# Kernel tuning notes

Hardware: AMD Instinct MI355X
Metric: run time of the kernel (lower is better)

## Reference

```python
import jax, jax.numpy as jnp
import numpy as np

B, L, D_IN = 4, 2048, 80
D, H, DFF, WIN = 128, 16, 128, 64
DH = D // H
BN_EPS = 1e-5


def sinusoidal_positional_encoding(l, d, dtype):
    # Faithful to source: pos_j = 10000 ** (j / d) (exponent j/d, not 2j/d)
    n = d // 2 + (d % 2 == 1)
    pos_i = jnp.arange(l, dtype=dtype)[:, None]                  # [L,1]
    pos_j = jnp.power(jnp.asarray(10000.0, dtype), jnp.arange(n, dtype=dtype) / d)  # [n]
    ang = pos_i / pos_j                                          # [L,n]
    pos = jnp.stack([jnp.sin(ang), jnp.cos(ang)], axis=-1).reshape(l, -1)
    return pos[:, :d]                                            # [L,D]


def local_window_disallowed_mask(l, win):
    # Source: mask starts as ones (True = disallowed), zeros only strictly
    i = jnp.arange(l)
    diff = jnp.abs(i[:, None] - i[None, :])
    allowed = (diff >= 1) & (diff <= win)
    return ~allowed                                              # [L,L] bool, True = masked


def setup_inputs() -> dict:
    key = jax.random.key(0)
    ks = jax.random.split(key, 17)
    s = 0.05  # weight scale for numerical stability
    return {
        "x": jax.random.normal(ks[0], (B, L, D_IN), jnp.float32),
        "conv_w": jax.random.normal(ks[1], (D, D_IN), jnp.float32) * s,
        "conv_b": jax.random.normal(ks[2], (D,), jnp.float32) * s,
        "bn_g": jax.random.uniform(ks[3], (D,), jnp.float32, 0.5, 1.5),
        "bn_b": jax.random.normal(ks[4], (D,), jnp.float32) * s,
        "bn_rm": jax.random.normal(ks[5], (D,), jnp.float32) * s,
        "bn_rv": jax.random.uniform(ks[6], (D,), jnp.float32, 0.5, 1.5),
        "in_proj_w": jax.random.normal(ks[7], (3 * D, D), jnp.float32) * s,
        "in_proj_b": jax.random.normal(ks[8], (3 * D,), jnp.float32) * s,
        "out_w": jax.random.normal(ks[9], (D, D), jnp.float32) * s,
        "out_b": jax.random.normal(ks[10], (D,), jnp.float32) * s,
        "ff_w1": jax.random.normal(ks[11], (DFF, D), jnp.float32) * s,
        "ff_b1": jax.random.normal(ks[12], (DFF,), jnp.float32) * s,
        "ff_w2": jax.random.normal(ks[13], (D, DFF), jnp.float32) * s,
        "ff_b2": jax.random.normal(ks[14], (D,), jnp.float32) * s,
        "fc_w": jax.random.normal(ks[15], (D_IN, D), jnp.float32) * s,
        "fc_b": jax.random.normal(ks[16], (D_IN,), jnp.float32) * s,
    }


def _forward(x, conv_w, conv_b, bn_g, bn_b, bn_rm, bn_rv,
             in_proj_w, in_proj_b, out_w, out_b,
             ff_w1, ff_b1, ff_w2, ff_b2, fc_w, fc_b):
    b, l, _ = x.shape
    dt = x.dtype
    # Conv1d(kernel=1) + ReLU + BatchNorm1d (eval mode, running stats)
    h = jax.nn.relu(jnp.einsum('bli,oi->blo', x, conv_w) + conv_b)     # [B,L,D]
    h = (h - bn_rm) * (bn_g * jax.lax.rsqrt(bn_rv + BN_EPS)) + bn_b
    # positional encoding
    h = h + sinusoidal_positional_encoding(l, D, dt)
    # MultiheadAttention (torch semantics: joint in_proj, scaled dot, out_proj)
    qkv = jnp.einsum('bld,ed->ble', h, in_proj_w) + in_proj_b          # [B,L,3D]
    q, k, v = jnp.split(qkv, 3, axis=-1)
    q = q.reshape(b, l, H, DH).transpose(0, 2, 1, 3)                   # [B,H,L,dh]
    k = k.reshape(b, l, H, DH).transpose(0, 2, 1, 3)
    v = v.reshape(b, l, H, DH).transpose(0, 2, 1, 3)
    scores = jnp.einsum('bhqd,bhkd->bhqk', q, k) / jnp.sqrt(jnp.asarray(DH, dt))
    mask = local_window_disallowed_mask(l, WIN)                        # True = masked
    scores = jnp.where(mask, jnp.finfo(dt).min, scores)
    attn = jax.nn.softmax(scores, axis=-1)                             # [B,H,L,L]
    ctx = jnp.einsum('bhqk,bhkd->bhqd', attn, v)
    ctx = ctx.transpose(0, 2, 1, 3).reshape(b, l, D)
    attn_out = jnp.einsum('bld,od->blo', ctx, out_w) + out_b           # [B,L,D]
    # FFN (no residual in source)
    f = jax.nn.relu(jnp.einsum('bld,fd->blf', attn_out, ff_w1) + ff_b1)
    f = jnp.einsum('blf,df->bld', f, ff_w2) + ff_b2                    # [B,L,D]
    # final head
    return jnp.einsum('bld,od->blo', f, fc_w) + fc_b                   # [B,L,80]


def reference(x, conv_w, conv_b, bn_g, bn_b, bn_rm, bn_rv,
              in_proj_w, in_proj_b, out_w, out_b,
              ff_w1, ff_b1, ff_w2, ff_b2, fc_w, fc_b):
    return _forward(x, conv_w, conv_b, bn_g, bn_b, bn_rm, bn_rv,
                    in_proj_w, in_proj_b, out_w, out_b,
                    ff_w1, ff_b1, ff_w2, ff_b2, fc_w, fc_b)
```

## Files before the change

### kernel.cpp

```cpp
#include <hip/hip_runtime.h>
#include <hip/hip_bf16.h>
#include <math.h>

constexpr int B_ = 4, L_ = 2048, DIN = 80, D_ = 128, H_ = 16, DH = 8;
constexpr int T_ = B_ * L_;
constexpr int LDX = T_;

__device__ float g_xT  [DIN * T_];
__device__ float g_posT[D_ * L_];
__device__ float g_h   [D_ * T_];
__device__ float g_ctx [D_ * T_];
__device__ float g_f1  [D_ * T_];
__device__ float g_q3  [B_ * H_ * L_ * DH];
__device__ float g_k3  [B_ * H_ * L_ * DH];
__device__ float g_v3  [B_ * H_ * L_ * DH];
__device__ float g_WconvT[DIN * D_];
__device__ float g_WqkvT [D_ * 3 * D_];
__device__ float g_Wf1T  [D_ * D_];
__device__ float g_WfcT  [D_ * D_];
__device__ float g_bf1   [D_];
__device__ float g_bfc   [D_];

__global__ void prep_fold(const float* __restrict__ x,
                          const float* __restrict__ conv_w,
                          const float* __restrict__ in_proj_w,
                          const float* __restrict__ out_w,
                          const float* __restrict__ out_b,
                          const float* __restrict__ ff_w1,
                          const float* __restrict__ ff_b1,
                          const float* __restrict__ ff_w2,
                          const float* __restrict__ ff_b2,
                          const float* __restrict__ fc_w,
                          const float* __restrict__ fc_b) {
    __shared__ float rowbuf[2][128];
    __shared__ float red[256];
    int bid = blockIdx.x, tid = threadIdx.x;

    if (bid < 512) {
        int idx = bid * 256 + tid;
        int l = idx >> 6, j = idx & 63;
        double ang = (double)l * exp((double)j * (-9.210340371976184 / 128.0));
        g_posT[(2 * j) * L_ + l]     = (float)sin(ang);
        g_posT[(2 * j + 1) * L_ + l] = (float)cos(ang);
        return;
    }
    if (bid < 3072) {
        int e = (bid - 512) * 256 + tid;
        int t = e / 80, k = e - t * 80;
        g_xT[k * T_ + t] = x[e];
        return;
    }
    if (bid < 3112) {
        int e = (bid - 3072) * 256 + tid;
        int o = e / 80, k = e - o * 80;
        g_WconvT[k * D_ + o] = conv_w[e];
        return;
    }
    if (bid < 3304) {
        int e = (bid - 3112) * 256 + tid;
        int o = e >> 7, k = e & 127;
        g_WqkvT[k * (3 * D_) + o] = in_proj_w[e];
        return;
    }
    if (bid < 3368) {
        int sub = tid >> 7, k = tid & 127;
        int f = (bid - 3304) * 2 + sub;
        rowbuf[sub][k] = ff_w1[f * 128 + k];
        __syncthreads();
        float acc = 0.f;
#pragma unroll 8
        for (int o = 0; o < 128; o++)
            acc = fmaf(rowbuf[sub][o], out_w[o * 128 + k], acc);
        g_Wf1T[k * 128 + f] = acc;
        red[tid] = rowbuf[sub][k] * out_b[k];
        __syncthreads();
        for (int s = 64; s > 0; s >>= 1) {
            if (k < s) red[tid] += red[tid + s];
            __syncthreads();
        }
        if (k == 0) g_bf1[f] = red[sub * 128] + ff_b1[f];
        return;
    }
    {
        int sub = tid >> 7, k = tid & 127;
        int o = (bid - 3368) * 2 + sub;
        rowbuf[sub][k] = (o < 80) ? fc_w[o * 128 + k] : 0.f;
        __syncthreads();
        float acc = 0.f;
#pragma unroll 8
        for (int d = 0; d < 128; d++)
            acc = fmaf(rowbuf[sub][d], ff_w2[d * 128 + k], acc);
        g_WfcT[k * 128 + o] = acc;
        red[tid] = rowbuf[sub][k] * ff_b2[k];
        __syncthreads();
        for (int s = 64; s > 0; s >>= 1) {
            if (k < s) red[tid] += red[tid + s];
            __syncthreads();
        }
        if (k == 0) g_bfc[o] = (o < 80) ? (red[sub * 128] + fc_b[o]) : 0.f;
        return;
    }
}

template <int K, int LDW, int EPI>
__global__ __launch_bounds__(256) void gemm_kernel(
        const float* __restrict__ X, const float* __restrict__ Wt,
        const float* __restrict__ bias,
        const float* __restrict__ bg, const float* __restrict__ bb,
        const float* __restrict__ brm, const float* __restrict__ brv,
        float* __restrict__ Y) {
    __shared__ float Xs[K][64];
    __shared__ float Ws[K][64];
    int tid = threadIdx.x;
    int t0 = blockIdx.x * 64;
    int cb = blockIdx.y * 64;
    int tc = tid & 15, tr = tid >> 4;

    for (int i = tid; i < K * 16; i += 256) {
        int k = i >> 4, f = i & 15;
        *(float4*)&Xs[k][f * 4] = *(const float4*)&X[(size_t)k * LDX + t0 + f * 4];
    }
    for (int i = tid; i < K * 16; i += 256) {
        int k = i >> 4, f = i & 15;
        *(float4*)&Ws[k][f * 4] = *(const float4*)&Wt[(size_t)k * LDW + cb + f * 4];
    }
    __syncthreads();

    float acc[4][4] = {};
#pragma unroll 4
    for (int k = 0; k < K; ++k) {
        float4 a = *(float4*)&Xs[k][tr * 4];
        float4 w = *(float4*)&Ws[k][tc * 4];
        float av[4] = {a.x, a.y, a.z, a.w};
        float wv[4] = {w.x, w.y, w.z, w.w};
#pragma unroll
        for (int i = 0; i < 4; i++)
#pragma unroll
            for (int jj = 0; jj < 4; jj++)
                acc[i][jj] = fmaf(av[i], wv[jj], acc[i][jj]);
    }

    if (EPI == 3) {
#pragma unroll
        for (int i = 0; i < 4; i++) {
            int t = t0 + tr * 4 + i;
            int b = t >> 11, l = t & 2047;
#pragma unroll
            for (int jj = 0; jj < 4; jj++) {
                int C = cb + tc * 4 + jj;
                float v = acc[i][jj] + bias[C];
                int slab = C >> 7, cs = C & 127;
                float* dst = (slab == 0) ? g_q3 : (slab == 1 ? g_k3 : g_v3);
                dst[(((size_t)(b * H_ + (cs >> 3))) * L_ + l) * DH + (cs & 7)] = v;
            }
        }
        return;
    }
    if (EPI == 4) {
#pragma unroll
        for (int i = 0; i < 4; i++) {
            int t = t0 + tr * 4 + i;
            int c0 = cb + tc * 4;
            if (c0 < 80) {
                float vs[4];
#pragma unroll
                for (int jj = 0; jj < 4; jj++) vs[jj] = acc[i][jj] + bias[c0 + jj];
                *(float4*)&Y[(size_t)t * 80 + c0] = *(float4*)vs;
            }
        }
        return;
    }
#pragma unroll
    for (int jj = 0; jj < 4; jj++) {
        int c = cb + tc * 4 + jj;
        float bv = bias[c];
        float vs[4];
#pragma unroll
        for (int i = 0; i < 4; i++) {
            float v = acc[i][jj] + bv;
            if (EPI == 1) v = fmaxf(v, 0.0f);
            if (EPI == 2) {
                v = fmaxf(v, 0.0f);
                v = (v - brm[c]) * (bg[c] * rsqrtf(brv[c] + 1e-5f)) + bb[c];
                v += g_posT[c * L_ + ((t0 + tr * 4) & 2047) + i];
            }
            vs[i] = v;
        }
        *(float4*)&Y[(size_t)c * LDX + t0 + tr * 4] = *(float4*)vs;
    }
}

__global__ __launch_bounds__(128) void attn_kernel() {
    __shared__ float Ks[385 * 8];
    __shared__ float Vs[385 * 8];
    int bh = blockIdx.x;
    int qb = blockIdx.y * 256;
    int tid = threadIdx.x;
    int kbase = qb - 64;

    const float* kgl = g_k3 + (size_t)bh * L_ * DH;
    const float* vgl = g_v3 + (size_t)bh * L_ * DH;
    const float* qgl = g_q3 + (size_t)bh * L_ * DH;

    for (int i = tid; i < 385 * 2; i += 128) {
        int li = i >> 1, half = i & 1;
        int j = kbase + li;
        float4 kf = {0, 0, 0, 0}, vf = {0, 0, 0, 0};
        if (j >= 0 && j < L_) {
            kf = *(const float4*)&kgl[j * 8 + half * 4];
            vf = *(const float4*)&vgl[j * 8 + half * 4];
        }
        *(float4*)&Ks[li * 8 + half * 4] = kf;
        *(float4*)&Vs[li * 8 + half * 4] = vf;
    }
    __syncthreads();

    const float sc = 0.35355339059327373f;
    int q0 = qb + 2 * tid;
    float qa[8], qc[8];
#pragma unroll
    for (int d = 0; d < 8; d++) {
        qa[d] = qgl[q0 * 8 + d] * sc;
        qc[d] = qgl[(q0 + 1) * 8 + d] * sc;
    }

    float l0 = 0.f, l1 = 0.f;
    float A0[8] = {}, A1[8] = {};
    int li0 = 2 * tid;
#pragma unroll 2
    for (int it = 0; it < 130; it++) {
        int li = li0 + it;
        int j = kbase + li;
        float kv[8], vv[8];
        *(float4*)kv       = *(float4*)&Ks[li * 8];
        *(float4*)(kv + 4) = *(float4*)&Ks[li * 8 + 4];
        *(float4*)vv       = *(float4*)&Vs[li * 8];
        *(float4*)(vv + 4) = *(float4*)&Vs[li * 8 + 4];
        float s0 = 0.f, s1 = 0.f;
#pragma unroll
        for (int d = 0; d < 8; d++) {
            s0 = fmaf(qa[d], kv[d], s0);
            s1 = fmaf(qc[d], kv[d], s1);
        }
        bool jv = (j >= 0) && (j < L_);
        bool ok0 = jv && (it != 64) && (it <= 128);
        bool ok1 = jv && (it != 65) && (it >= 1);
        float w0 = ok0 ? __expf(s0) : 0.f;
        float w1 = ok1 ? __expf(s1) : 0.f;
        l0 += w0; l1 += w1;
#pragma unroll
        for (int d = 0; d < 8; d++) {
            A0[d] = fmaf(w0, vv[d], A0[d]);
            A1[d] = fmaf(w1, vv[d], A1[d]);
        }
    }
    float i0 = 1.f / l0, i1 = 1.f / l1;
    int b = bh >> 4, h = bh & 15;
    int tb = b * L_ + q0;
#pragma unroll
    for (int d = 0; d < 8; d++) {
        g_ctx[(size_t)(h * 8 + d) * LDX + tb]     = A0[d] * i0;
        g_ctx[(size_t)(h * 8 + d) * LDX + tb + 1] = A1[d] * i1;
    }
}

extern "C" void kernel_launch(void* const* d_in, const int* in_sizes, int n_in,
                              void* d_out, int out_size, void* d_ws, size_t ws_size,
                              hipStream_t stream) {
    const float* x         = (const float*)d_in[0];
    const float* conv_w    = (const float*)d_in[1];
    const float* conv_b    = (const float*)d_in[2];
    const float* bn_g      = (const float*)d_in[3];
    const float* bn_b      = (const float*)d_in[4];
    const float* bn_rm     = (const float*)d_in[5];
    const float* bn_rv     = (const float*)d_in[6];
    const float* in_proj_w = (const float*)d_in[7];
    const float* in_proj_b = (const float*)d_in[8];
    const float* out_w     = (const float*)d_in[9];
    const float* out_b     = (const float*)d_in[10];
    const float* ff_w1     = (const float*)d_in[11];
    const float* ff_b1     = (const float*)d_in[12];
    const float* ff_w2     = (const float*)d_in[13];
    const float* ff_b2     = (const float*)d_in[14];
    const float* fc_w      = (const float*)d_in[15];
    const float* fc_b      = (const float*)d_in[16];

    float *p_xT, *p_h, *p_ctx, *p_f1, *p_WconvT, *p_WqkvT, *p_Wf1T, *p_WfcT, *p_bf1, *p_bfc;
    hipGetSymbolAddress((void**)&p_xT,     HIP_SYMBOL(g_xT));
    hipGetSymbolAddress((void**)&p_h,      HIP_SYMBOL(g_h));
    hipGetSymbolAddress((void**)&p_ctx,    HIP_SYMBOL(g_ctx));
    hipGetSymbolAddress((void**)&p_f1,     HIP_SYMBOL(g_f1));
    hipGetSymbolAddress((void**)&p_WconvT, HIP_SYMBOL(g_WconvT));
    hipGetSymbolAddress((void**)&p_WqkvT,  HIP_SYMBOL(g_WqkvT));
    hipGetSymbolAddress((void**)&p_Wf1T,   HIP_SYMBOL(g_Wf1T));
    hipGetSymbolAddress((void**)&p_WfcT,   HIP_SYMBOL(g_WfcT));
    hipGetSymbolAddress((void**)&p_bf1,    HIP_SYMBOL(g_bf1));
    hipGetSymbolAddress((void**)&p_bfc,    HIP_SYMBOL(g_bfc));

    prep_fold<<<3432, 256, 0, stream>>>(x, conv_w, in_proj_w, out_w, out_b,
                                        ff_w1, ff_b1, ff_w2, ff_b2, fc_w, fc_b);

    gemm_kernel<80, 128, 2><<<dim3(128, 2), 256, 0, stream>>>(
        p_xT, p_WconvT, conv_b, bn_g, bn_b, bn_rm, bn_rv, p_h);

    gemm_kernel<128, 384, 3><<<dim3(128, 6), 256, 0, stream>>>(
        p_h, p_WqkvT, in_proj_b, nullptr, nullptr, nullptr, nullptr, nullptr);

    attn_kernel<<<dim3(64, 8), 128, 0, stream>>>();

    gemm_kernel<128, 128, 1><<<dim3(128, 2), 256, 0, stream>>>(
        p_ctx, p_Wf1T, p_bf1, nullptr, nullptr, nullptr, nullptr, p_f1);

    gemm_kernel<128, 128, 4><<<dim3(128, 2), 256, 0, stream>>>(
        p_f1, p_WfcT, p_bfc, nullptr, nullptr, nullptr, nullptr, (float*)d_out);
}
```

Measured before the change: 175.5 us.

## Split attention window across two blocks, retile GEMMs, tiled transpose in prep

The attention kernel now splits each query's key window into a left and a right half, each handled by its own block, and writes partial sums that a new combine kernel adds and normalises. QKV is stored channel-major in one buffer and gathered per head into shared memory. The GEMMs gain K-chunking and narrower column tiles, which launches more blocks. The prep kernel uses a shared-memory tiled transpose for x and float positional encoding with fewer blocks. The cost is an extra kernel launch plus round-trips of the partial results through global memory, along with strided gathers of the QKV data.

```diff
diff --git a/kernel.cpp b/kernel.cpp
--- a/kernel.cpp
+++ b/kernel.cpp
@@ -5,15 +5,16 @@
 constexpr int B_ = 4, L_ = 2048, DIN = 80, D_ = 128, H_ = 16, DH = 8;
 constexpr int T_ = B_ * L_;
 constexpr int LDX = T_;
+constexpr int BHL = B_ * H_ * L_;
 
 __device__ float g_xT  [DIN * T_];
 __device__ float g_posT[D_ * L_];
 __device__ float g_h   [D_ * T_];
+__device__ float g_qkv [3 * D_ * T_];
 __device__ float g_ctx [D_ * T_];
 __device__ float g_f1  [D_ * T_];
-__device__ float g_q3  [B_ * H_ * L_ * DH];
-__device__ float g_k3  [B_ * H_ * L_ * DH];
-__device__ float g_v3  [B_ * H_ * L_ * DH];
+__device__ float g_pA  [2 * 8 * BHL];
+__device__ float g_pl  [2 * BHL];
 __device__ float g_WconvT[DIN * D_];
 __device__ float g_WqkvT [D_ * 3 * D_];
 __device__ float g_Wf1T  [D_ * D_];
@@ -21,58 +22,64 @@
 __device__ float g_bf1   [D_];
 __device__ float g_bfc   [D_];
 
-__global__ void prep_fold(const float* __restrict__ x,
-                          const float* __restrict__ conv_w,
-                          const float* __restrict__ in_proj_w,
-                          const float* __restrict__ out_w,
-                          const float* __restrict__ out_b,
-                          const float* __restrict__ ff_w1,
-                          const float* __restrict__ ff_b1,
-                          const float* __restrict__ ff_w2,
-                          const float* __restrict__ ff_b2,
-                          const float* __restrict__ fc_w,
-                          const float* __restrict__ fc_b) {
-    __shared__ float rowbuf[2][128];
-    __shared__ float red[256];
+__global__ __launch_bounds__(256) void prep_kernel(
+        const float* __restrict__ x,
+        const float* __restrict__ conv_w,
+        const float* __restrict__ in_proj_w,
+        const float* __restrict__ out_w,  const float* __restrict__ out_b,
+        const float* __restrict__ ff_w1,  const float* __restrict__ ff_b1,
+        const float* __restrict__ ff_w2,  const float* __restrict__ ff_b2,
+        const float* __restrict__ fc_w,   const float* __restrict__ fc_b) {
+    __shared__ float smem[80 * 65];
     int bid = blockIdx.x, tid = threadIdx.x;
 
-    if (bid < 512) {
-        int idx = bid * 256 + tid;
+    if (bid < 128) {
+        int t0 = bid * 64;
+        for (int i = tid; i < 64 * 80; i += 256) {
+            int t = i / 80, k = i - t * 80;
+            smem[k * 65 + t] = x[(size_t)(t0) * 80 + i];
+        }
+        __syncthreads();
+        for (int i = tid; i < 80 * 64; i += 256) {
+            int k = i >> 6, tt = i & 63;
+            g_xT[(size_t)k * T_ + t0 + tt] = smem[k * 65 + tt];
+        }
+        return;
+    }
+    if (bid < 640) {
+        int idx = (bid - 128) * 256 + tid;
         int l = idx >> 6, j = idx & 63;
-        double ang = (double)l * exp((double)j * (-9.210340371976184 / 128.0));
-        g_posT[(2 * j) * L_ + l]     = (float)sin(ang);
-        g_posT[(2 * j + 1) * L_ + l] = (float)cos(ang);
-        return;
-    }
-    if (bid < 3072) {
-        int e = (bid - 512) * 256 + tid;
-        int t = e / 80, k = e - t * 80;
-        g_xT[k * T_ + t] = x[e];
-        return;
-    }
-    if (bid < 3112) {
-        int e = (bid - 3072) * 256 + tid;
+        float inv = __expf((float)j * (-9.210340371976184f / 128.0f));
+        float ang = (float)l * inv;
+        g_posT[(2 * j) * L_ + l]     = sinf(ang);
+        g_posT[(2 * j + 1) * L_ + l] = cosf(ang);
+        return;
+    }
+    if (bid < 680) {
+        int e = (bid - 640) * 256 + tid;
         int o = e / 80, k = e - o * 80;
         g_WconvT[k * D_ + o] = conv_w[e];
         return;
     }
-    if (bid < 3304) {
-        int e = (bid - 3112) * 256 + tid;
+    if (bid < 872) {
+        int e = (bid - 680) * 256 + tid;
         int o = e >> 7, k = e & 127;
         g_WqkvT[k * (3 * D_) + o] = in_proj_w[e];
         return;
     }
-    if (bid < 3368) {
+    float* rowbuf = smem;
+    float* red = smem + 256;
+    if (bid < 936) {
         int sub = tid >> 7, k = tid & 127;
-        int f = (bid - 3304) * 2 + sub;
-        rowbuf[sub][k] = ff_w1[f * 128 + k];
+        int f = (bid - 872) * 2 + sub;
+        rowbuf[sub * 128 + k] = ff_w1[f * 128 + k];
         __syncthreads();
         float acc = 0.f;
 #pragma unroll 8
         for (int o = 0; o < 128; o++)
-            acc = fmaf(rowbuf[sub][o], out_w[o * 128 + k], acc);
+            acc = fmaf(rowbuf[sub * 128 + o], out_w[o * 128 + k], acc);
         g_Wf1T[k * 128 + f] = acc;
-        red[tid] = rowbuf[sub][k] * out_b[k];
+        red[tid] = rowbuf[sub * 128 + k] * out_b[k];
         __syncthreads();
         for (int s = 64; s > 0; s >>= 1) {
             if (k < s) red[tid] += red[tid + s];
@@ -83,15 +90,15 @@
     }
     {
         int sub = tid >> 7, k = tid & 127;
-        int o = (bid - 3368) * 2 + sub;
-        rowbuf[sub][k] = (o < 80) ? fc_w[o * 128 + k] : 0.f;
+        int o = (bid - 936) * 2 + sub;
+        rowbuf[sub * 128 + k] = (o < 80) ? fc_w[o * 128 + k] : 0.f;
         __syncthreads();
         float acc = 0.f;
 #pragma unroll 8
         for (int d = 0; d < 128; d++)
-            acc = fmaf(rowbuf[sub][d], ff_w2[d * 128 + k], acc);
+            acc = fmaf(rowbuf[sub * 128 + d], ff_w2[d * 128 + k], acc);
         g_WfcT[k * 128 + o] = acc;
-        red[tid] = rowbuf[sub][k] * ff_b2[k];
+        red[tid] = rowbuf[sub * 128 + k] * ff_b2[k];
         __syncthreads();
         for (int s = 64; s > 0; s >>= 1) {
             if (k < s) red[tid] += red[tid + s];
@@ -102,77 +109,68 @@
     }
 }
 
-template <int K, int LDW, int EPI>
+template <int K, int BK, int BN, int LDW, int EPI>
 __global__ __launch_bounds__(256) void gemm_kernel(
         const float* __restrict__ X, const float* __restrict__ Wt,
         const float* __restrict__ bias,
         const float* __restrict__ bg, const float* __restrict__ bb,
         const float* __restrict__ brm, const float* __restrict__ brv,
         float* __restrict__ Y) {
-    __shared__ float Xs[K][64];
-    __shared__ float Ws[K][64];
+    constexpr int TN = BN / 16;
+    __shared__ float Xs[BK][64];
+    __shared__ float Ws[BK][BN];
     int tid = threadIdx.x;
     int t0 = blockIdx.x * 64;
-    int cb = blockIdx.y * 64;
+    int cb = blockIdx.y * BN;
     int tc = tid & 15, tr = tid >> 4;
 
-    for (int i = tid; i < K * 16; i += 256) {
-        int k = i >> 4, f = i & 15;
-        *(float4*)&Xs[k][f * 4] = *(const float4*)&X[(size_t)k * LDX + t0 + f * 4];
-    }
-    for (int i = tid; i < K * 16; i += 256) {
-        int k = i >> 4, f = i & 15;
-        *(float4*)&Ws[k][f * 4] = *(const float4*)&Wt[(size_t)k * LDW + cb + f * 4];
-    }
-    __syncthreads();
-
-    float acc[4][4] = {};
+    float acc[4][TN] = {};
+    for (int kc = 0; kc < K; kc += BK) {
+        for (int i = tid; i < BK * 16; i += 256) {
+            int k = i >> 4, f = i & 15;
+            *(float4*)&Xs[k][f * 4] =
+                *(const float4*)&X[(size_t)(kc + k) * LDX + t0 + f * 4];
+        }
+        for (int i = tid; i < BK * (BN / 4); i += 256) {
+            int k = i / (BN / 4), f = i - k * (BN / 4);
+            *(float4*)&Ws[k][f * 4] =
+                *(const float4*)&Wt[(size_t)(kc + k) * LDW + cb + f * 4];
+        }
+        __syncthreads();
 #pragma unroll 4
-    for (int k = 0; k < K; ++k) {
-        float4 a = *(float4*)&Xs[k][tr * 4];
-        float4 w = *(float4*)&Ws[k][tc * 4];
-        float av[4] = {a.x, a.y, a.z, a.w};
-        float wv[4] = {w.x, w.y, w.z, w.w};
-#pragma unroll
-        for (int i = 0; i < 4; i++)
-#pragma unroll
-            for (int jj = 0; jj < 4; jj++)
-                acc[i][jj] = fmaf(av[i], wv[jj], acc[i][jj]);
-    }
-
-    if (EPI == 3) {
-#pragma unroll
-        for (int i = 0; i < 4; i++) {
-            int t = t0 + tr * 4 + i;
-            int b = t >> 11, l = t & 2047;
-#pragma unroll
-            for (int jj = 0; jj < 4; jj++) {
-                int C = cb + tc * 4 + jj;
-                float v = acc[i][jj] + bias[C];
-                int slab = C >> 7, cs = C & 127;
-                float* dst = (slab == 0) ? g_q3 : (slab == 1 ? g_k3 : g_v3);
-                dst[(((size_t)(b * H_ + (cs >> 3))) * L_ + l) * DH + (cs & 7)] = v;
+        for (int k = 0; k < BK; ++k) {
+            float4 a = *(float4*)&Xs[k][tr * 4];
+            float av[4] = {a.x, a.y, a.z, a.w};
+            float wv[TN];
+#pragma unroll
+            for (int jj = 0; jj < TN; jj++) wv[jj] = Ws[k][tc * TN + jj];
+#pragma unroll
+            for (int i = 0; i < 4; i++)
+#pragma unroll
+                for (int jj = 0; jj < TN; jj++)
+                    acc[i][jj] = fmaf(av[i], wv[jj], acc[i][jj]);
+        }
+        __syncthreads();
+    }
+
+    if (EPI == 4) {
+#pragma unroll
+        for (int jj = 0; jj < TN; jj++) {
+            int c = cb + tc * TN + jj;
+            if (c < 80) {
+                float bv = bias[c];
+#pragma unroll
+                for (int i = 0; i < 4; i++) {
+                    int t = t0 + tr * 4 + i;
+                    Y[(size_t)t * 80 + c] = acc[i][jj] + bv;
+                }
             }
         }
         return;
     }
-    if (EPI == 4) {
-#pragma unroll
-        for (int i = 0; i < 4; i++) {
-            int t = t0 + tr * 4 + i;
-            int c0 = cb + tc * 4;
-            if (c0 < 80) {
-                float vs[4];
-#pragma unroll
-                for (int jj = 0; jj < 4; jj++) vs[jj] = acc[i][jj] + bias[c0 + jj];
-                *(float4*)&Y[(size_t)t * 80 + c0] = *(float4*)vs;
-            }
-        }
-        return;
-    }
-#pragma unroll
-    for (int jj = 0; jj < 4; jj++) {
-        int c = cb + tc * 4 + jj;
+#pragma unroll
+    for (int jj = 0; jj < TN; jj++) {
+        int c = cb + tc * TN + jj;
         float bv = bias[c];
         float vs[4];
 #pragma unroll
@@ -182,7 +180,7 @@
             if (EPI == 2) {
                 v = fmaxf(v, 0.0f);
                 v = (v - brm[c]) * (bg[c] * rsqrtf(brv[c] + 1e-5f)) + bb[c];
-                v += g_posT[c * L_ + ((t0 + tr * 4) & 2047) + i];
+                v += g_posT[c * L_ + ((t0 & 2047) + tr * 4 + i)];
             }
             vs[i] = v;
         }
@@ -191,76 +189,93 @@
 }
 
 __global__ __launch_bounds__(128) void attn_kernel() {
-    __shared__ float Ks[385 * 8];
-    __shared__ float Vs[385 * 8];
-    int bh = blockIdx.x;
-    int qb = blockIdx.y * 256;
+    __shared__ float4 SK[2][2][160];
+    __shared__ float4 SV[2][2][160];
+    int bh = blockIdx.x, tile = blockIdx.y, hf = blockIdx.z;
+    int b = bh >> 4, h = bh & 15;
+    int qb = tile * 256;
     int tid = threadIdx.x;
-    int kbase = qb - 64;
-
-    const float* kgl = g_k3 + (size_t)bh * L_ * DH;
-    const float* vgl = g_v3 + (size_t)bh * L_ * DH;
-    const float* qgl = g_q3 + (size_t)bh * L_ * DH;
-
-    for (int i = tid; i < 385 * 2; i += 128) {
-        int li = i >> 1, half = i & 1;
-        int j = kbase + li;
-        float4 kf = {0, 0, 0, 0}, vf = {0, 0, 0, 0};
-        if (j >= 0 && j < L_) {
-            kf = *(const float4*)&kgl[j * 8 + half * 4];
-            vf = *(const float4*)&vgl[j * 8 + half * 4];
-        }
-        *(float4*)&Ks[li * 8 + half * 4] = kf;
-        *(float4*)&Vs[li * 8 + half * 4] = vf;
+    int jbase = hf ? (qb + 1) : (qb - 64);
+    int tb = b * L_;
+
+    for (int c16 = 0; c16 < 16; c16++) {
+        int d = (c16 < 8) ? c16 : (c16 - 8);
+        int ch = ((c16 < 8) ? 128 : 256) + h * 8 + d;
+        const float* src = g_qkv + (size_t)ch * LDX + tb;
+        for (int s = tid; s < 319; s += 128) {
+            int j = jbase + s;
+            float v = ((unsigned)j < (unsigned)L_) ? src[j] : 0.f;
+            float4* arr = (c16 < 8) ? &SK[s & 1][d >> 2][s >> 1]
+                                    : &SV[s & 1][d >> 2][s >> 1];
+            ((float*)arr)[d & 3] = v;
+        }
     }
     __syncthreads();
 
     const float sc = 0.35355339059327373f;
     int q0 = qb + 2 * tid;
     float qa[8], qc[8];
-#pragma unroll
-    for (int d = 0; d < 8; d++) {
-        qa[d] = qgl[q0 * 8 + d] * sc;
-        qc[d] = qgl[(q0 + 1) * 8 + d] * sc;
+    {
+        const float* qsrc = g_qkv + tb;
+#pragma unroll
+        for (int d = 0; d < 8; d++) {
+            qa[d] = qsrc[(size_t)(h * 8 + d) * LDX + q0] * sc;
+            qc[d] = qsrc[(size_t)(h * 8 + d) * LDX + q0 + 1] * sc;
+        }
     }
 
     float l0 = 0.f, l1 = 0.f;
     float A0[8] = {}, A1[8] = {};
-    int li0 = 2 * tid;
-#pragma unroll 2
-    for (int it = 0; it < 130; it++) {
-        int li = li0 + it;
-        int j = kbase + li;
-        float kv[8], vv[8];
-        *(float4*)kv       = *(float4*)&Ks[li * 8];
-        *(float4*)(kv + 4) = *(float4*)&Ks[li * 8 + 4];
-        *(float4*)vv       = *(float4*)&Vs[li * 8];
-        *(float4*)(vv + 4) = *(float4*)&Vs[li * 8 + 4];
+    int j00 = jbase + 2 * tid;
+
+    auto step = [&](int it, bool m0, bool m1) {
+        int p = it & 1, idx = tid + (it >> 1);
+        float4 ka = SK[p][0][idx], kb = SK[p][1][idx];
+        float kv[8] = {ka.x, ka.y, ka.z, ka.w, kb.x, kb.y, kb.z, kb.w};
         float s0 = 0.f, s1 = 0.f;
 #pragma unroll
         for (int d = 0; d < 8; d++) {
             s0 = fmaf(qa[d], kv[d], s0);
             s1 = fmaf(qc[d], kv[d], s1);
         }
-        bool jv = (j >= 0) && (j < L_);
-        bool ok0 = jv && (it != 64) && (it <= 128);
-        bool ok1 = jv && (it != 65) && (it >= 1);
-        float w0 = ok0 ? __expf(s0) : 0.f;
-        float w1 = ok1 ? __expf(s1) : 0.f;
+        bool jv = (unsigned)(j00 + it) < (unsigned)L_;
+        float w0 = (m0 && jv) ? __expf(s0) : 0.f;
+        float w1 = (m1 && jv) ? __expf(s1) : 0.f;
         l0 += w0; l1 += w1;
+        float4 va = SV[p][0][idx], vb = SV[p][1][idx];
+        float vv[8] = {va.x, va.y, va.z, va.w, vb.x, vb.y, vb.z, vb.w};
 #pragma unroll
         for (int d = 0; d < 8; d++) {
             A0[d] = fmaf(w0, vv[d], A0[d]);
             A1[d] = fmaf(w1, vv[d], A1[d]);
         }
-    }
-    float i0 = 1.f / l0, i1 = 1.f / l1;
+    };
+
+    step(0, true, false);
+#pragma unroll 2
+    for (int it = 1; it <= 63; it++) step(it, true, true);
+    step(64, false, true);
+
+    int base = bh * L_ + q0;
+#pragma unroll
+    for (int d = 0; d < 8; d++) {
+        g_pA[(hf * 8 + d) * BHL + base]     = A0[d];
+        g_pA[(hf * 8 + d) * BHL + base + 1] = A1[d];
+    }
+    g_pl[hf * BHL + base]     = l0;
+    g_pl[hf * BHL + base + 1] = l1;
+}
+
+__global__ __launch_bounds__(256) void combine_kernel() {
+    int gq = blockIdx.x * 256 + threadIdx.x;
+    int bh = gq >> 11, l = gq & 2047;
     int b = bh >> 4, h = bh & 15;
-    int tb = b * L_ + q0;
+    float ls = g_pl[gq] + g_pl[BHL + gq];
+    float inv = 1.f / ls;
 #pragma unroll
     for (int d = 0; d < 8; d++) {
-        g_ctx[(size_t)(h * 8 + d) * LDX + tb]     = A0[d] * i0;
-        g_ctx[(size_t)(h * 8 + d) * LDX + tb + 1] = A1[d] * i1;
+        float v = (g_pA[d * BHL + gq] + g_pA[(8 + d) * BHL + gq]) * inv;
+        g_ctx[(size_t)(h * 8 + d) * LDX + b * L_ + l] = v;
     }
 }
 
@@ -285,9 +300,11 @@
     const float* fc_w      = (const float*)d_in[15];
     const float* fc_b      = (const float*)d_in[16];
 
-    float *p_xT, *p_h, *p_ctx, *p_f1, *p_WconvT, *p_WqkvT, *p_Wf1T, *p_WfcT, *p_bf1, *p_bfc;
+    float *p_xT, *p_h, *p_qkv, *p_ctx, *p_f1;
+    float *p_WconvT, *p_WqkvT, *p_Wf1T, *p_WfcT, *p_bf1, *p_bfc;
     hipGetSymbolAddress((void**)&p_xT,     HIP_SYMBOL(g_xT));
     hipGetSymbolAddress((void**)&p_h,      HIP_SYMBOL(g_h));
+    hipGetSymbolAddress((void**)&p_qkv,    HIP_SYMBOL(g_qkv));
     hipGetSymbolAddress((void**)&p_ctx,    HIP_SYMBOL(g_ctx));
     hipGetSymbolAddress((void**)&p_f1,     HIP_SYMBOL(g_f1));
     hipGetSymbolAddress((void**)&p_WconvT, HIP_SYMBOL(g_WconvT));
@@ -297,20 +314,21 @@
     hipGetSymbolAddress((void**)&p_bf1,    HIP_SYMBOL(g_bf1));
     hipGetSymbolAddress((void**)&p_bfc,    HIP_SYMBOL(g_bfc));
 
-    prep_fold<<<3432, 256, 0, stream>>>(x, conv_w, in_proj_w, out_w, out_b,
-                                        ff_w1, ff_b1, ff_w2, ff_b2, fc_w, fc_b);
-
-    gemm_kernel<80, 128, 2><<<dim3(128, 2), 256, 0, stream>>>(
+    prep_kernel<<<1000, 256, 0, stream>>>(x, conv_w, in_proj_w, out_w, out_b,
+                                          ff_w1, ff_b1, ff_w2, ff_b2, fc_w, fc_b);
+
+    gemm_kernel<80, 80, 32, 128, 2><<<dim3(128, 4), 256, 0, stream>>>(
         p_xT, p_WconvT, conv_b, bn_g, bn_b, bn_rm, bn_rv, p_h);
 
-    gemm_kernel<128, 384, 3><<<dim3(128, 6), 256, 0, stream>>>(
-        p_h, p_WqkvT, in_proj_b, nullptr, nullptr, nullptr, nullptr, nullptr);
-
-    attn_kernel<<<dim3(64, 8), 128, 0, stream>>>();
-
-    gemm_kernel<128, 128, 1><<<dim3(128, 2), 256, 0, stream>>>(
+    gemm_kernel<128, 64, 64, 384, 0><<<dim3(128, 6), 256, 0, stream>>>(
+        p_h, p_WqkvT, in_proj_b, nullptr, nullptr, nullptr, nullptr, p_qkv);
+
+    attn_kernel<<<dim3(64, 8, 2), 128, 0, stream>>>();
+    combine_kernel<<<512, 256, 0, stream>>>();
+
+    gemm_kernel<128, 128, 32, 128, 1><<<dim3(128, 4), 256, 0, stream>>>(
         p_ctx, p_Wf1T, p_bf1, nullptr, nullptr, nullptr, nullptr, p_f1);
 
-    gemm_kernel<128, 128, 4><<<dim3(128, 2), 256, 0, stream>>>(
+    gemm_kernel<128, 128, 32, 128, 4><<<dim3(128, 3), 256, 0, stream>>>(
         p_f1, p_WfcT, p_bfc, nullptr, nullptr, nullptr, nullptr, (float*)d_out);
 }
```

Result: faster. 164.4 us (-6.3%).
